# Optimization experiments

Measured on AMD Instinct MI355X. Metric: run time of the kernel, lower is better.

Reference implementation:

```python
import jax, jax.numpy as jnp
import numpy as np
from jax import lax

T, D, HID, C = 16384, 1024, 1024, 16
H = HID // 2  # per-direction hidden size


def _uniform(key, shape, bound):
    return jax.random.uniform(key, shape, jnp.float32, -bound, bound)


def setup_inputs() -> dict:
    key = jax.random.key(0)
    ks = jax.random.split(key, 16)
    s = 1.0 / np.sqrt(H)        # PyTorch LSTM init bound
    sl = 1.0 / np.sqrt(HID)     # PyTorch Linear init bound
    return {
        "sequence": jax.random.normal(ks[0], (T, D), jnp.float32),
        "h0": jax.random.normal(ks[1], (2, 1, H), jnp.float32),
        "c0": jax.random.normal(ks[2], (2, 1, H), jnp.float32),
        "w_ih_f": _uniform(ks[3], (4 * H, D), s),
        "w_hh_f": _uniform(ks[4], (4 * H, H), s),
        "b_ih_f": _uniform(ks[5], (4 * H,), s),
        "b_hh_f": _uniform(ks[6], (4 * H,), s),
        "w_ih_b": _uniform(ks[7], (4 * H, D), s),
        "w_hh_b": _uniform(ks[8], (4 * H, H), s),
        "b_ih_b": _uniform(ks[9], (4 * H,), s),
        "b_hh_b": _uniform(ks[10], (4 * H,), s),
        "w_lin": _uniform(ks[11], (C, HID), sl),
        "b_lin": _uniform(ks[12], (C,), sl),
        "transitions": jax.random.uniform(ks[13], (C, C), jnp.float32),  # torch.rand
    }


def _lstm_scan(x, h0, c0, w_ih, w_hh, b_ih, b_hh, reverse):
    # x: [T, D]; PyTorch gate order: i, f, g, o
    def step(carry, xt):
        h, c = carry
        g = w_ih @ xt + b_ih + w_hh @ h + b_hh  # [4H]
        i, f, gg, o = jnp.split(g, 4)
        i = jax.nn.sigmoid(i)
        f = jax.nn.sigmoid(f)
        gg = jnp.tanh(gg)
        o = jax.nn.sigmoid(o)
        c = f * c + i * gg
        h = o * jnp.tanh(c)
        return (h, c), h
    _, hs = lax.scan(step, (h0, c0), x, reverse=reverse)
    return hs  # [T, H], hs[t] = hidden at time t (aligned for both directions)


def _viterbi(feats, transitions):
    # feats: [T, C]; init forward_var = zeros (per the original torch.full(..., 0))
    def vstep(fv, feat):
        scores = fv[None, :] + transitions          # [C_next, C_prev]
        bp = jnp.argmax(scores, axis=1)             # backpointers
        fv2 = jnp.max(scores, axis=1) + feat
        return fv2, bp
    fv, bps = lax.scan(vstep, jnp.zeros((C,), feats.dtype), feats)
    best = jnp.argmax(fv)
    path_score = fv[best]
    def bstep(b, bp_row):
        nb = bp_row[b]
        return nb, nb
    _, rev = lax.scan(bstep, best, bps, reverse=True)  # rev[t] = state before step t's transition
    best_path = jnp.concatenate([rev, best[None]])     # length T+1, matches torch output
    return path_score, best_path


def reference(sequence, h0, c0, w_ih_f, w_hh_f, b_ih_f, b_hh_f,
              w_ih_b, w_hh_b, b_ih_b, b_hh_b, w_lin, b_lin, transitions):
    hs_f = _lstm_scan(sequence, h0[0, 0], c0[0, 0], w_ih_f, w_hh_f, b_ih_f, b_hh_f, False)
    hs_b = _lstm_scan(sequence, h0[1, 0], c0[1, 0], w_ih_b, w_hh_b, b_ih_b, b_hh_b, True)
    lstm_out = jnp.concatenate([hs_f, hs_b], axis=-1)   # [T, HID]
    feats = lstm_out @ w_lin.T + b_lin                  # [T, C]
    return _viterbi(feats, transitions)
```

## Files before the change

### kernel.cpp

```cpp
#include <hip/hip_runtime.h>

#define T_STEPS 16384
#define CSTEPS  1024
#define NCHUNK  16
#define DMODEL  1024
#define HID     512
#define G4      2048
#define NC      16
#define NGEMMB  128

#define POLL_GUARD (1 << 16)

static const size_t OFF_Z     = 0;
static const size_t OFF_HF    = 8388608ull;
static const size_t OFF_HB    = 16777216ull;
static const size_t OFF_FEATS = 25165824ull;
static const size_t FLOATS_TOTAL = 25427968ull;
static const size_t OFF_BP_B  = FLOATS_TOTAL * 4ull;
static const size_t OFF_P_B   = OFF_BP_B + 262144ull;
static const size_t OFF_EX_B  = OFF_P_B + 262144ull;
static const size_t OFF_CTR_B = OFF_EX_B + 16384ull;
static const size_t NEED_B    = OFF_CTR_B + 1024ull;

__device__ __forceinline__ float sigm_fast(float x) { return 1.0f / (1.0f + __expf(-x)); }
__device__ __forceinline__ float tanh_fast(float x) { return 1.0f - 2.0f / (__expf(2.0f * x) + 1.0f); }

__global__ __launch_bounds__(256, 1) void fused_kernel(
    const float* __restrict__ seq,
    const float* __restrict__ wih_f, const float* __restrict__ bih_f, const float* __restrict__ bhh_f,
    const float* __restrict__ wih_b, const float* __restrict__ bih_b, const float* __restrict__ bhh_b,
    const float* __restrict__ whh_f, const float* __restrict__ whh_b,
    const float* __restrict__ h0, const float* __restrict__ c0,
    float* __restrict__ hf, float* __restrict__ hb,
    float* __restrict__ Zbuf,
    unsigned long long* __restrict__ exf,
    unsigned int* __restrict__ gemm_done, unsigned int* __restrict__ recur_prog)
{
    const int bid = blockIdx.x;
    const int tid = threadIdx.x;
    const int pk  = bid & 7;

    __shared__ float pad_lds[24576];
    if (gemm_done == recur_prog) {
        ((volatile float*)pad_lds)[tid] = 1.0f;
    }

    if (pk < 2) {
        const int dir = pk;
        const int g   = bid >> 3;
        const float* whh = dir ? whh_b : whh_f;
        float* hout      = dir ? hb : hf;
        unsigned long long* ex = dir ? (exf + 1024) : exf;

        const int w = tid >> 6, lane = tid & 63;
        const int G = lane >> 4, u = lane & 15;
        const int R = 512 * G + 16 * g + u;

        float wreg[128];
        {
            const float* src = &whh[(size_t)R * HID + w * 128];
            #pragma unroll
            for (int j = 0; j < 32; ++j) {
                float4 v = *(const float4*)&src[j * 4];
                wreg[j*4+0]=v.x; wreg[j*4+1]=v.y; wreg[j*4+2]=v.z; wreg[j*4+3]=v.w;
            }
        }

        __shared__ __align__(16) float h_lds[512];
        __shared__ __align__(16) float p_lds[2][256];
        __shared__ int cntl[8];
        __shared__ int deadf;

        if (tid < 8) cntl[tid] = -1;
        if (tid == 8) deadf = 0;
        __syncthreads();

        volatile int* vcnt  = (volatile int*)cntl;
        volatile int* vdead = (volatile int*)&deadf;

        float cst = 0.f;
        if (w == 0 && lane < 16) cst = c0[dir * HID + 16 * g + lane];

        {
            const int i0 = 128 * w + 2 * lane;
            h_lds[i0]     = h0[dir * HID + i0];
            h_lds[i0 + 1] = h0[dir * HID + i0 + 1];
        }

        int dead = 0;
        const float* Zd = Zbuf + (size_t)dir * 2 * CSTEPS * G4;
        float zr_cur = 0.f, zr_pref = 0.f;

        for (int s = 0; s < T_STEPS; ++s) {
            const int par = s & 1;

            if (w == 1) {
                if ((s & (CSTEPS - 1)) == 0) {
                    const int cg = s >> 10;
                    int guard = 0; unsigned int gd;
                    for (;;) {
                        gd = __hip_atomic_load(&gemm_done[cg], __ATOMIC_RELAXED,
                                               __HIP_MEMORY_SCOPE_AGENT);
                        if (gd >= (unsigned)NGEMMB) break;
                        __builtin_amdgcn_s_sleep(2);
                        if (++guard > (1 << 16)) { dead = 1; break; }
                    }
                    const int rr = dir ? (1023 - (s & 1023)) : (s & 1023);
                    zr_cur = __hip_atomic_load(
                        &Zd[((size_t)((s >> 10) & 1) * CSTEPS + rr) * G4 + R],
                        __ATOMIC_RELAXED, __HIP_MEMORY_SCOPE_AGENT);
                } else {
                    zr_cur = zr_pref;
                }
            }

            if (s > 0) {
                const int i0   = 128 * w + 2 * lane;
                const int base = par * 512 + i0;
                const unsigned long long want = (unsigned long long)(unsigned)s;
                unsigned long long v0, v1;
                int guard = 0;
                for (;;) {
                    v0 = __hip_atomic_load(&ex[base],     __ATOMIC_RELAXED, __HIP_MEMORY_SCOPE_AGENT);
                    v1 = __hip_atomic_load(&ex[base + 1], __ATOMIC_RELAXED, __HIP_MEMORY_SCOPE_AGENT);
                    if (((v0 >> 32) == want) & ((v1 >> 32) == want)) break;
                    if ((++guard & 63) == 0) {
                        if (*vdead) { dead = 1; break; }
                        if (guard > POLL_GUARD) { *vdead = 1; dead = 1; break; }
                    }
                }
                union { unsigned int ui; float f; } ca, cb;
                ca.ui = (unsigned int)v0; cb.ui = (unsigned int)v1;
                h_lds[i0]     = ca.f;
                h_lds[i0 + 1] = cb.f;
            }
            if (dead) { *vdead = 1; break; }

            float a0 = 0.f, a1 = 0.f, a2 = 0.f, a3 = 0.f;
            {
                const float4* h4 = (const float4*)&h_lds[w * 128];
                #pragma unroll
                for (int j = 0; j < 8; ++j) {
                    float4 h_0 = h4[4*j+0], h_1 = h4[4*j+1], h_2 = h4[4*j+2], h_3 = h4[4*j+3];
                    a0 += wreg[16*j+ 0]*h_0.x + wreg[16*j+ 1]*h_0.y + wreg[16*j+ 2]*h_0.z + wreg[16*j+ 3]*h_0.w;
                    a1 += wreg[16*j+ 4]*h_1.x + wreg[16*j+ 5]*h_1.y + wreg[16*j+ 6]*h_1.z + wreg[16*j+ 7]*h_1.w;
                    a2 += wreg[16*j+ 8]*h_2.x + wreg[16*j+ 9]*h_2.y + wreg[16*j+10]*h_2.z + wreg[16*j+11]*h_2.w;
                    a3 += wreg[16*j+12]*h_3.x + wreg[16*j+13]*h_3.y + wreg[16*j+14]*h_3.z + wreg[16*j+15]*h_3.w;
                }
            }
            float acc = (a0 + a1) + (a2 + a3);

            if (w != 0) {
                if (w == 1) {
                    acc += zr_cur;
                    if (((s + 1) & (CSTEPS - 1)) != 0) {
                        const int sn = s + 1;
                        const int rr = dir ? (1023 - (sn & 1023)) : (sn & 1023);
                        zr_pref = __hip_atomic_load(
                            &Zd[((size_t)((sn >> 10) & 1) * CSTEPS + rr) * G4 + R],
                            __ATOMIC_RELAXED, __HIP_MEMORY_SCOPE_AGENT);
                    }
                }
                p_lds[par][64 * w + lane] = acc;
                asm volatile("s_waitcnt lgkmcnt(0)" ::: "memory");
                if (lane == 0) vcnt[par * 4 + w] = s;
            } else {
                int guard = 0;
                for (;;) {
                    int c1 = vcnt[par * 4 + 1];
                    int c2 = vcnt[par * 4 + 2];
                    int c3 = vcnt[par * 4 + 3];
                    if ((c1 == s) & (c2 == s) & (c3 == s)) break;
                    if ((++guard & 63) == 0) {
                        if (*vdead) { dead = 1; break; }
                        if (guard > (1 << 16)) { *vdead = 1; dead = 1; break; }
                    }
                }
                if (dead) break;
                float rv = acc + p_lds[par][64 + lane]
                         + p_lds[par][128 + lane] + p_lds[par][192 + lane];
                float a = (G == 2) ? tanh_fast(rv) : sigm_fast(rv);
                float ig = __shfl(a, u,      64);
                float fg = __shfl(a, u + 16, 64);
                float gg = __shfl(a, u + 32, 64);
                float og = __shfl(a, u + 48, 64);
                if (lane < 16) {
                    float cn = fg * cst + ig * gg;
                    cst = cn;
                    float hn = og * tanh_fast(cn);
                    union { float f; unsigned int ui; } cv; cv.f = hn;
                    unsigned long long pv =
                        ((unsigned long long)(unsigned)(s + 1) << 32) | (unsigned long long)cv.ui;
                    __hip_atomic_store(&ex[((s + 1) & 1) * 512 + 16 * g + lane], pv,
                                       __ATOMIC_RELAXED, __HIP_MEMORY_SCOPE_AGENT);
                    const int t = dir ? (T_STEPS - 1 - s) : s;
                    hout[(size_t)t * HID + 16 * g + lane] = hn;
                }
                if ((s & (CSTEPS - 1)) == (CSTEPS - 1) && lane == 0)
                    __hip_atomic_fetch_add(&recur_prog[s >> 10], 1u, __ATOMIC_RELAXED,
                                           __HIP_MEMORY_SCOPE_AGENT);
            }
        }
        if (dead) *vdead = 1;
    } else if (pk < 6) {
        const int gb = (pk - 2) * 32 + (bid >> 3);
        __shared__ __align__(16) float As[16][68];
        __shared__ __align__(16) float Bs[16][68];
        const int lr = tid >> 2, ls = tid & 3, tx = tid & 15, ty = tid >> 4;

        for (int cc = 0; cc < NCHUNK; ++cc) {
            if (cc >= 2 && tid == 0) {
                int guard = 0; unsigned int rp;
                for (;;) {
                    rp = __hip_atomic_load(&recur_prog[cc - 2], __ATOMIC_RELAXED,
                                           __HIP_MEMORY_SCOPE_AGENT);
                    if (rp >= 64u) break;
                    __builtin_amdgcn_s_sleep(16);
                    if (++guard > (1 << 14)) break;
                }
            }
            __syncthreads();

            for (int tix = gb; tix < 2 * 16 * 32; tix += NGEMMB) {
                const int dr  = tix >> 9;
                const int rem = tix & 511;
                const int mt  = rem >> 5;
                const int nt  = rem & 31;
                const int t0  = dr ? (T_STEPS - (cc + 1) * CSTEPS) : (cc * CSTEPS);
                const float* W  = dr ? wih_b : wih_f;
                const float* bi = dr ? bih_b : bih_f;
                const float* bh = dr ? bhh_b : bhh_f;
                float* Zt = Zbuf + (size_t)(dr * 2 + (cc & 1)) * CSTEPS * G4;

                float acc[4][4] = {};
                for (int k0 = 0; k0 < DMODEL; k0 += 16) {
                    float4 av = *(const float4*)&seq[(size_t)(t0 + mt*64 + lr) * DMODEL + k0 + ls*4];
                    float4 bv = *(const float4*)&W[(size_t)(nt*64 + lr) * DMODEL + k0 + ls*4];
                    __syncthreads();
                    As[ls*4+0][lr]=av.x; As[ls*4+1][lr]=av.y; As[ls*4+2][lr]=av.z; As[ls*4+3][lr]=av.w;
                    Bs[ls*4+0][lr]=bv.x; Bs[ls*4+1][lr]=bv.y; Bs[ls*4+2][lr]=bv.z; Bs[ls*4+3][lr]=bv.w;
                    __syncthreads();
                    #pragma unroll
                    for (int k = 0; k < 16; ++k) {
                        float4 a = *(const float4*)&As[k][ty * 4];
                        float4 b = *(const float4*)&Bs[k][tx * 4];
                        acc[0][0]+=a.x*b.x; acc[0][1]+=a.x*b.y; acc[0][2]+=a.x*b.z; acc[0][3]+=a.x*b.w;
                        acc[1][0]+=a.y*b.x; acc[1][1]+=a.y*b.y; acc[1][2]+=a.y*b.z; acc[1][3]+=a.y*b.w;
                        acc[2][0]+=a.z*b.x; acc[2][1]+=a.z*b.y; acc[2][2]+=a.z*b.z; acc[2][3]+=a.z*b.w;
                        acc[3][0]+=a.w*b.x; acc[3][1]+=a.w*b.y; acc[3][2]+=a.w*b.z; acc[3][3]+=a.w*b.w;
                    }
                }
                float4 b4  = *(const float4*)&bi[nt * 64 + tx * 4];
                float4 c4v = *(const float4*)&bh[nt * 64 + tx * 4];
                float bx=b4.x+c4v.x, by=b4.y+c4v.y, bz=b4.z+c4v.z, bw_=b4.w+c4v.w;
                #pragma unroll
                for (int i = 0; i < 4; ++i) {
                    float4 o;
                    o.x=acc[i][0]+bx; o.y=acc[i][1]+by; o.z=acc[i][2]+bz; o.w=acc[i][3]+bw_;
                    *(float4*)&Zt[(size_t)(mt*64 + ty*4 + i) * G4 + nt*64 + tx*4] = o;
                }
            }
            __threadfence();
            __syncthreads();
            if (tid == 0)
                __hip_atomic_fetch_add(&gemm_done[cc], 1u, __ATOMIC_RELEASE,
                                       __HIP_MEMORY_SCOPE_AGENT);
        }
    }
}

__global__ __launch_bounds__(256) void feats_kernel(
    const float* __restrict__ hf, const float* __restrict__ hb,
    const float* __restrict__ wlin, const float* __restrict__ blin,
    float* __restrict__ feats)
{
    const int t = blockIdx.x;
    __shared__ __align__(16) float hl[1024];
    const int tid = threadIdx.x;
    {
        const float* src = (tid < 128) ? &hf[(size_t)t * HID + tid * 4]
                                       : &hb[(size_t)t * HID + (tid - 128) * 4];
        *(float4*)&hl[tid * 4] = *(const float4*)src;
    }
    __syncthreads();
    const int c = tid >> 4, p = tid & 15;
    float s = 0.0f;
    #pragma unroll
    for (int j = 0; j < 16; ++j) {
        float4 h4 = *(const float4*)&hl[p * 4 + j * 64];
        float4 w4 = *(const float4*)&wlin[(size_t)c * 1024 + p * 4 + j * 64];
        s += h4.x*w4.x + h4.y*w4.y + h4.z*w4.z + h4.w*w4.w;
    }
    s += __shfl_down(s, 8, 16);
    s += __shfl_down(s, 4, 16);
    s += __shfl_down(s, 2, 16);
    s += __shfl_down(s, 1, 16);
    if (p == 0) feats[t * NC + c] = s + blin[c];
}

__global__ __launch_bounds__(64) void viterbi_kernel(
    const float* __restrict__ feats, const float* __restrict__ trans,
    unsigned char* __restrict__ bp, float* __restrict__ out,
    unsigned int* __restrict__ bT)
{
    __shared__ __align__(16) float fl[4096];
    __shared__ __align__(16) float fvs[16];
    const int l = threadIdx.x;
    float tr[16];
    if (l < 16) {
        #pragma unroll
        for (int j = 0; j < 16; ++j) tr[j] = trans[l * 16 + j];
    }
    float fv = 0.0f;
    for (int cb = 0; cb < 64; ++cb) {
        #pragma unroll
        for (int j = 0; j < 16; ++j)
            *(float4*)&fl[j * 256 + l * 4] =
                *(const float4*)&feats[cb * 4096 + j * 256 + l * 4];
        __syncthreads();
        if (l < 16) {
            for (int k = 0; k < 256; ++k) {
                float m = __shfl(fv, 0, 16) + tr[0];
                int bi = 0;
                #pragma unroll
                for (int j = 1; j < 16; ++j) {
                    float sc = __shfl(fv, j, 16) + tr[j];
                    if (sc > m) { m = sc; bi = j; }
                }
                bp[(size_t)(cb * 256 + k) * 16 + l] = (unsigned char)bi;
                fv = m + fl[k * 16 + l];
            }
        }
        __syncthreads();
    }
    if (l < 16) fvs[l] = fv;
    __syncthreads();
    if (l == 0) {
        float best = fvs[0]; int bi = 0;
        #pragma unroll
        for (int j = 1; j < 16; ++j) if (fvs[j] > best) { best = fvs[j]; bi = j; }
        out[0] = best;
        out[1 + T_STEPS] = (float)bi;
        *bT = (unsigned int)bi;
    }
}

__global__ __launch_bounds__(64) void maps_kernel(
    const unsigned char* __restrict__ bp, unsigned char* __restrict__ P)
{
    const int j = blockIdx.x;
    const int l = threadIdx.x;
    __shared__ __align__(16) unsigned char lb[4096];
    __shared__ __align__(16) unsigned char lp[4096];
    #pragma unroll
    for (int i = 0; i < 4; ++i)
        *(uint4*)&lb[i * 1024 + l * 16] = *(const uint4*)&bp[(size_t)j * 4096 + i * 1024 + l * 16];
    __syncthreads();
    if (l < 16) {
        int cur = l;
        for (int k = 255; k >= 0; --k) {
            cur = lb[k * 16 + cur];
            lp[k * 16 + l] = (unsigned char)cur;
        }
    }
    __syncthreads();
    #pragma unroll
    for (int i = 0; i < 4; ++i)
        *(uint4*)&P[(size_t)j * 4096 + i * 1024 + l * 16] = *(const uint4*)&lp[i * 1024 + l * 16];
}

__global__ __launch_bounds__(64) void path_kernel(
    const unsigned char* __restrict__ P, const unsigned int* __restrict__ bT,
    float* __restrict__ out)
{
    const int j = blockIdx.x;
    const int l = threadIdx.x;
    int e = (int)(*bT);
    for (int i = 63; i > j; --i) e = P[(size_t)i * 4096 + e];
    for (int k = l; k < 256; k += 64)
        out[1 + j * 256 + k] = (float)P[(size_t)j * 4096 + k * 16 + e];
}

__global__ void fb_kernel(float* out, int n, float v0) {
    int i = blockIdx.x * 256 + threadIdx.x;
    if (i < n) out[i] = (i == 0) ? v0 : 0.0f;
}

extern "C" void kernel_launch(void* const* d_in, const int* in_sizes, int n_in,
                              void* d_out, int out_size, void* d_ws, size_t ws_size,
                              hipStream_t stream) {
    const float* seq   = (const float*)d_in[0];
    const float* h0    = (const float*)d_in[1];
    const float* c0    = (const float*)d_in[2];
    const float* wih_f = (const float*)d_in[3];
    const float* whh_f = (const float*)d_in[4];
    const float* bih_f = (const float*)d_in[5];
    const float* bhh_f = (const float*)d_in[6];
    const float* wih_b = (const float*)d_in[7];
    const float* whh_b = (const float*)d_in[8];
    const float* bih_b = (const float*)d_in[9];
    const float* bhh_b = (const float*)d_in[10];
    const float* wlin  = (const float*)d_in[11];
    const float* blin  = (const float*)d_in[12];
    const float* trans = (const float*)d_in[13];
    float* out = (float*)d_out;

    if (ws_size < NEED_B) {
        fb_kernel<<<(out_size + 255) / 256, 256, 0, stream>>>(out, out_size, -(float)ws_size);
        return;
    }

    float* wsf = (float*)d_ws;
    float* Zbuf  = wsf + OFF_Z;
    float* hf    = wsf + OFF_HF;
    float* hb    = wsf + OFF_HB;
    float* feats = wsf + OFF_FEATS;
    unsigned char* bp = (unsigned char*)d_ws + OFF_BP_B;
    unsigned char* P  = (unsigned char*)d_ws + OFF_P_B;
    unsigned long long* exf = (unsigned long long*)((char*)d_ws + OFF_EX_B);
    unsigned int* ctr = (unsigned int*)((char*)d_ws + OFF_CTR_B);
    unsigned int* gemm_done  = ctr;
    unsigned int* recur_prog = ctr + 16;
    unsigned int* bT         = ctr + 32;

    hipMemsetAsync((void*)exf, 0, 16384 + 1024, stream);

    {
        void* args[] = { (void*)&seq,
                         (void*)&wih_f, (void*)&bih_f, (void*)&bhh_f,
                         (void*)&wih_b, (void*)&bih_b, (void*)&bhh_b,
                         (void*)&whh_f, (void*)&whh_b,
                         (void*)&h0, (void*)&c0,
                         (void*)&hf, (void*)&hb, (void*)&Zbuf,
                         (void*)&exf,
                         (void*)&gemm_done, (void*)&recur_prog };
        hipError_t e = hipLaunchCooperativeKernel(
            reinterpret_cast<void*>(fused_kernel), dim3(256), dim3(256),
            args, 0, stream);
        if (e != hipSuccess) {
            fused_kernel<<<256, 256, 0, stream>>>(
                seq, wih_f, bih_f, bhh_f, wih_b, bih_b, bhh_b,
                whh_f, whh_b, h0, c0, hf, hb, Zbuf, exf,
                gemm_done, recur_prog);
        }
    }

    feats_kernel<<<16384, 256, 0, stream>>>(hf, hb, wlin, blin, feats);
    viterbi_kernel<<<1, 64, 0, stream>>>(feats, trans, bp, out, bT);
    maps_kernel<<<64, 64, 0, stream>>>(bp, P);
    path_kernel<<<64, 64, 0, stream>>>(P, bT, out);
}
```

Before: 46.55 ms.

## Give each recurrent wave its own hidden units and reduce with shuffles

The recurrent work is repartitioned so each of the four waves in a block owns four hidden units with all four gates, and splits the 512-wide dot product across the four 16-lane quarters of the wave. Partial sums are combined with xor-shuffles instead of LDS partials collected by wave 0. This removes the serial wave-0 bottleneck that waited on three producer waves and then did all activations alone. In exchange every wave now publishes h into a double-buffered LDS array and spins on an all-wave LDS tag barrier each step, and the progress counter now expects 256 wave arrivals instead of 64.

```diff
diff --git a/kernel.cpp b/kernel.cpp
--- a/kernel.cpp
+++ b/kernel.cpp
@@ -8,8 +8,10 @@
 #define G4      2048
 #define NC      16
 #define NGEMMB  128
+#define RWAVES  256u
 
 #define POLL_GUARD (1 << 16)
+#define LDS_GUARD  (1 << 17)
 
 static const size_t OFF_Z     = 0;
 static const size_t OFF_HF    = 8388608ull;
@@ -52,40 +54,37 @@
         float* hout      = dir ? hb : hf;
         unsigned long long* ex = dir ? (exf + 1024) : exf;
 
-        const int w = tid >> 6, lane = tid & 63;
-        const int G = lane >> 4, u = lane & 15;
-        const int R = 512 * G + 16 * g + u;
+        const int w    = tid >> 6, lane = tid & 63;
+        const int rl   = lane & 15;
+        const int q    = lane >> 4;
+        const int Gg   = rl >> 2;
+        const int v    = rl & 3;
+        const int unit = 16 * g + 4 * w + v;
+        const int R    = 512 * Gg + unit;
 
         float wreg[128];
         {
-            const float* src = &whh[(size_t)R * HID + w * 128];
+            const float* src = &whh[(size_t)R * HID + q * 128];
             #pragma unroll
             for (int j = 0; j < 32; ++j) {
-                float4 v = *(const float4*)&src[j * 4];
-                wreg[j*4+0]=v.x; wreg[j*4+1]=v.y; wreg[j*4+2]=v.z; wreg[j*4+3]=v.w;
-            }
-        }
-
-        __shared__ __align__(16) float h_lds[512];
-        __shared__ __align__(16) float p_lds[2][256];
-        __shared__ int cntl[8];
+                float4 x = *(const float4*)&src[j * 4];
+                wreg[j*4+0]=x.x; wreg[j*4+1]=x.y; wreg[j*4+2]=x.z; wreg[j*4+3]=x.w;
+            }
+        }
+
+        __shared__ __align__(16) float h_sh[2][512];
+        __shared__ int qtag[2][4];
         __shared__ int deadf;
 
-        if (tid < 8) cntl[tid] = -1;
+        if (tid < 8) ((volatile int*)qtag)[tid] = -1;
         if (tid == 8) deadf = 0;
         __syncthreads();
 
-        volatile int* vcnt  = (volatile int*)cntl;
+        volatile int* vtag  = (volatile int*)qtag;
         volatile int* vdead = (volatile int*)&deadf;
 
         float cst = 0.f;
-        if (w == 0 && lane < 16) cst = c0[dir * HID + 16 * g + lane];
-
-        {
-            const int i0 = 128 * w + 2 * lane;
-            h_lds[i0]     = h0[dir * HID + i0];
-            h_lds[i0 + 1] = h0[dir * HID + i0 + 1];
-        }
+        if (lane < 4) cst = c0[dir * HID + unit];
 
         int dead = 0;
         const float* Zd = Zbuf + (size_t)dir * 2 * CSTEPS * G4;
@@ -94,51 +93,75 @@
         for (int s = 0; s < T_STEPS; ++s) {
             const int par = s & 1;
 
-            if (w == 1) {
-                if ((s & (CSTEPS - 1)) == 0) {
-                    const int cg = s >> 10;
-                    int guard = 0; unsigned int gd;
-                    for (;;) {
-                        gd = __hip_atomic_load(&gemm_done[cg], __ATOMIC_RELAXED,
-                                               __HIP_MEMORY_SCOPE_AGENT);
-                        if (gd >= (unsigned)NGEMMB) break;
-                        __builtin_amdgcn_s_sleep(2);
-                        if (++guard > (1 << 16)) { dead = 1; break; }
-                    }
+            if ((s & (CSTEPS - 1)) == 0) {
+                const int cg = s >> 10;
+                int guard = 0; unsigned int gd;
+                for (;;) {
+                    gd = __hip_atomic_load(&gemm_done[cg], __ATOMIC_RELAXED,
+                                           __HIP_MEMORY_SCOPE_AGENT);
+                    if (gd >= (unsigned)NGEMMB) break;
+                    __builtin_amdgcn_s_sleep(2);
+                    if (++guard > (1 << 16)) { dead = 1; break; }
+                }
+                if (lane < 16) {
                     const int rr = dir ? (1023 - (s & 1023)) : (s & 1023);
                     zr_cur = __hip_atomic_load(
                         &Zd[((size_t)((s >> 10) & 1) * CSTEPS + rr) * G4 + R],
                         __ATOMIC_RELAXED, __HIP_MEMORY_SCOPE_AGENT);
+                }
+            }
+
+            {
+                const int i0 = 128 * w + 2 * lane;
+                float hv0, hv1;
+                if (s == 0) {
+                    hv0 = h0[dir * HID + i0];
+                    hv1 = h0[dir * HID + i0 + 1];
                 } else {
-                    zr_cur = zr_pref;
-                }
-            }
-
-            if (s > 0) {
-                const int i0   = 128 * w + 2 * lane;
-                const int base = par * 512 + i0;
-                const unsigned long long want = (unsigned long long)(unsigned)s;
-                unsigned long long v0, v1;
+                    const int base = par * 512 + i0;
+                    const unsigned long long want = (unsigned long long)(unsigned)s;
+                    unsigned long long v0, v1;
+                    int guard = 0;
+                    for (;;) {
+                        v0 = __hip_atomic_load(&ex[base],     __ATOMIC_RELAXED, __HIP_MEMORY_SCOPE_AGENT);
+                        v1 = __hip_atomic_load(&ex[base + 1], __ATOMIC_RELAXED, __HIP_MEMORY_SCOPE_AGENT);
+                        if (((v0 >> 32) == want) & ((v1 >> 32) == want)) break;
+                        if ((++guard & 63) == 0) {
+                            if (*vdead) { dead = 1; break; }
+                            if (guard > POLL_GUARD) { *vdead = 1; dead = 1; break; }
+                        }
+                    }
+                    union { unsigned int ui; float f; } ca, cb;
+                    ca.ui = (unsigned int)v0; cb.ui = (unsigned int)v1;
+                    hv0 = ca.f; hv1 = cb.f;
+                }
+                if (dead) { *vdead = 1; break; }
+                h_sh[par][i0]     = hv0;
+                h_sh[par][i0 + 1] = hv1;
+                asm volatile("s_waitcnt lgkmcnt(0)" ::: "memory");
+                if (lane == 0) vtag[par * 4 + w] = s;
+            }
+
+            {
                 int guard = 0;
                 for (;;) {
-                    v0 = __hip_atomic_load(&ex[base],     __ATOMIC_RELAXED, __HIP_MEMORY_SCOPE_AGENT);
-                    v1 = __hip_atomic_load(&ex[base + 1], __ATOMIC_RELAXED, __HIP_MEMORY_SCOPE_AGENT);
-                    if (((v0 >> 32) == want) & ((v1 >> 32) == want)) break;
+                    int c0f = vtag[par * 4 + 0];
+                    int c1f = vtag[par * 4 + 1];
+                    int c2f = vtag[par * 4 + 2];
+                    int c3f = vtag[par * 4 + 3];
+                    if ((c0f == s) & (c1f == s) & (c2f == s) & (c3f == s)) break;
                     if ((++guard & 63) == 0) {
                         if (*vdead) { dead = 1; break; }
-                        if (guard > POLL_GUARD) { *vdead = 1; dead = 1; break; }
+                        if (guard > LDS_GUARD) { *vdead = 1; dead = 1; break; }
                     }
                 }
-                union { unsigned int ui; float f; } ca, cb;
-                ca.ui = (unsigned int)v0; cb.ui = (unsigned int)v1;
-                h_lds[i0]     = ca.f;
-                h_lds[i0 + 1] = cb.f;
-            }
-            if (dead) { *vdead = 1; break; }
+                if (dead) break;
+                asm volatile("" ::: "memory");
+            }
 
             float a0 = 0.f, a1 = 0.f, a2 = 0.f, a3 = 0.f;
             {
-                const float4* h4 = (const float4*)&h_lds[w * 128];
+                const float4* h4 = (const float4*)&h_sh[par][q * 128];
                 #pragma unroll
                 for (int j = 0; j < 8; ++j) {
                     float4 h_0 = h4[4*j+0], h_1 = h4[4*j+1], h_2 = h4[4*j+2], h_3 = h4[4*j+3];
@@ -149,57 +172,41 @@
                 }
             }
             float acc = (a0 + a1) + (a2 + a3);
-
-            if (w != 0) {
-                if (w == 1) {
-                    acc += zr_cur;
-                    if (((s + 1) & (CSTEPS - 1)) != 0) {
-                        const int sn = s + 1;
-                        const int rr = dir ? (1023 - (sn & 1023)) : (sn & 1023);
-                        zr_pref = __hip_atomic_load(
-                            &Zd[((size_t)((sn >> 10) & 1) * CSTEPS + rr) * G4 + R],
-                            __ATOMIC_RELAXED, __HIP_MEMORY_SCOPE_AGENT);
-                    }
-                }
-                p_lds[par][64 * w + lane] = acc;
-                asm volatile("s_waitcnt lgkmcnt(0)" ::: "memory");
-                if (lane == 0) vcnt[par * 4 + w] = s;
-            } else {
-                int guard = 0;
-                for (;;) {
-                    int c1 = vcnt[par * 4 + 1];
-                    int c2 = vcnt[par * 4 + 2];
-                    int c3 = vcnt[par * 4 + 3];
-                    if ((c1 == s) & (c2 == s) & (c3 == s)) break;
-                    if ((++guard & 63) == 0) {
-                        if (*vdead) { dead = 1; break; }
-                        if (guard > (1 << 16)) { *vdead = 1; dead = 1; break; }
-                    }
-                }
-                if (dead) break;
-                float rv = acc + p_lds[par][64 + lane]
-                         + p_lds[par][128 + lane] + p_lds[par][192 + lane];
-                float a = (G == 2) ? tanh_fast(rv) : sigm_fast(rv);
-                float ig = __shfl(a, u,      64);
-                float fg = __shfl(a, u + 16, 64);
-                float gg = __shfl(a, u + 32, 64);
-                float og = __shfl(a, u + 48, 64);
-                if (lane < 16) {
-                    float cn = fg * cst + ig * gg;
-                    cst = cn;
-                    float hn = og * tanh_fast(cn);
-                    union { float f; unsigned int ui; } cv; cv.f = hn;
-                    unsigned long long pv =
-                        ((unsigned long long)(unsigned)(s + 1) << 32) | (unsigned long long)cv.ui;
-                    __hip_atomic_store(&ex[((s + 1) & 1) * 512 + 16 * g + lane], pv,
-                                       __ATOMIC_RELAXED, __HIP_MEMORY_SCOPE_AGENT);
-                    const int t = dir ? (T_STEPS - 1 - s) : s;
-                    hout[(size_t)t * HID + 16 * g + lane] = hn;
-                }
-                if ((s & (CSTEPS - 1)) == (CSTEPS - 1) && lane == 0)
-                    __hip_atomic_fetch_add(&recur_prog[s >> 10], 1u, __ATOMIC_RELAXED,
-                                           __HIP_MEMORY_SCOPE_AGENT);
-            }
+            if (q == 0) acc += zr_cur;
+
+            if (lane < 16 && ((s + 1) & (CSTEPS - 1)) != 0) {
+                const int sn = s + 1;
+                const int rr = dir ? (1023 - (sn & 1023)) : (sn & 1023);
+                zr_pref = __hip_atomic_load(
+                    &Zd[((size_t)((sn >> 10) & 1) * CSTEPS + rr) * G4 + R],
+                    __ATOMIC_RELAXED, __HIP_MEMORY_SCOPE_AGENT);
+            }
+
+            acc += __shfl_xor(acc, 16, 64);
+            acc += __shfl_xor(acc, 32, 64);
+
+            float a = (Gg == 2) ? tanh_fast(acc) : sigm_fast(acc);
+            float ig = __shfl(a,  v,      64);
+            float fg = __shfl(a,  4 + v,  64);
+            float gg = __shfl(a,  8 + v,  64);
+            float og = __shfl(a, 12 + v,  64);
+            if (lane < 4) {
+                float cn = fg * cst + ig * gg;
+                cst = cn;
+                float hn = og * tanh_fast(cn);
+                union { float f; unsigned int ui; } cv; cv.f = hn;
+                unsigned long long pv =
+                    ((unsigned long long)(unsigned)(s + 1) << 32) | (unsigned long long)cv.ui;
+                __hip_atomic_store(&ex[((s + 1) & 1) * 512 + unit], pv,
+                                   __ATOMIC_RELAXED, __HIP_MEMORY_SCOPE_AGENT);
+                const int t = dir ? (T_STEPS - 1 - s) : s;
+                hout[(size_t)t * HID + unit] = hn;
+            }
+            if (lane < 16) zr_cur = zr_pref;
+
+            if ((s & (CSTEPS - 1)) == (CSTEPS - 1) && lane == 0)
+                __hip_atomic_fetch_add(&recur_prog[s >> 10], 1u, __ATOMIC_RELAXED,
+                                       __HIP_MEMORY_SCOPE_AGENT);
         }
         if (dead) *vdead = 1;
     } else if (pk < 6) {
@@ -214,7 +221,7 @@
                 for (;;) {
                     rp = __hip_atomic_load(&recur_prog[cc - 2], __ATOMIC_RELAXED,
                                            __HIP_MEMORY_SCOPE_AGENT);
-                    if (rp >= 64u) break;
+                    if (rp >= RWAVES) break;
                     __builtin_amdgcn_s_sleep(16);
                     if (++guard > (1 << 14)) break;
                 }
```

New measurement: 64.84 ms. 1.39x slower.
